# Kernel optimization log

Hardware: AMD Instinct MI355X
Metric: run time of the kernel (lower is better)

The kernel has to match this reference:

```python
import jax, jax.numpy as jnp
import numpy as np

NEG = -1e4      # BigBird additive mask value
LN_EPS = 1e-12  # BERT-style LayerNorm eps


def _bigbird_forward(xs_pad, mask, Wq, bq, Wk, bk, Wv, bv, Wo, bo, gamma, beta, rand_idx):
    b, n, hsz = xs_pad.shape
    H = rand_idx.shape[0]
    nb = rand_idx.shape[1] + 2          # one rand row per non-edge query block
    BS = n // nb                        # block size
    d = hsz // H
    r = rand_idx.shape[2]
    scale = 1.0 / np.sqrt(d).astype(np.float32)

    mf = mask.reshape(b, n).astype(xs_pad.dtype)   # (b,n) 1=token, 0=pad
    mb = mf.reshape(b, nb, BS)                     # blocked mask

    def proj(W, bias):
        return (xs_pad @ W + bias).reshape(b, n, H, d).transpose(0, 2, 1, 3)

    q = proj(Wq, bq) * scale            # (b,H,n,d)
    k = proj(Wk, bk)
    v = proj(Wv, bv)
    qb = q.reshape(b, H, nb, BS, d)
    kb = k.reshape(b, H, nb, BS, d)
    vb = v.reshape(b, H, nb, BS, d)

    # ---- global rows: first / last query block attend to all keys ----
    def full_row(qi):                   # qi: (b,H,BS,d)
        s = jnp.einsum('bhqd,bhkd->bhqk', qi, k) + (1.0 - mf)[:, None, None, :] * NEG
        return jnp.einsum('bhqk,bhkd->bhqd', jax.nn.softmax(s, axis=-1), v)

    ctx_first = full_row(qb[:, :, 0])
    ctx_last = full_row(qb[:, :, nb - 1])

    # ---- random key/value blocks: per-head, per-query-block gather ----
    hidx = jnp.arange(H)[:, None, None]
    rand_k = kb[:, hidx, rand_idx].reshape(b, H, nb - 2, r * BS, d)
    rand_v = vb[:, hidx, rand_idx].reshape(b, H, nb - 2, r * BS, d)
    rand_m = mb[:, rand_idx].reshape(b, H, nb - 2, r * BS)

    def sparse_row(qi, kc, vc, mc):     # kc:(b,H,K,d), mc:(b,H,K)
        s = jnp.einsum('bhqd,bhkd->bhqk', qi, kc) + (1.0 - mc)[:, :, None, :] * NEG
        return jnp.einsum('bhqk,bhkd->bhqd', jax.nn.softmax(s, axis=-1), vc)

    def gather_blocks(ids, ridx):
        kc = jnp.concatenate([kb[:, :, j] for j in ids] + [rand_k[:, :, ridx]], axis=2)
        vc = jnp.concatenate([vb[:, :, j] for j in ids] + [rand_v[:, :, ridx]], axis=2)
        mc = jnp.concatenate([jnp.broadcast_to(mb[:, None, j], (b, H, BS)) for j in ids]
                             + [rand_m[:, :, ridx]], axis=2)
        return kc, vc, mc

    # second / penultimate query blocks: window + globals + rand
    ctx_second = sparse_row(qb[:, :, 1], *gather_blocks([0, 1, 2, nb - 1], 0))
    ctx_penult = sparse_row(qb[:, :, nb - 2], *gather_blocks([nb - 3, nb - 2, nb - 1, 0], nb - 3))

    # ---- middle rows i in [2, nb-3]: 3-block sliding window + first/last global + r random ----
    nmid = nb - 4
    mid = jnp.arange(2, nb - 2)
    win = mid[:, None] + jnp.arange(-1, 2)[None, :]        # (nmid,3)
    k_win = kb[:, :, win].reshape(b, H, nmid, 3 * BS, d)
    v_win = vb[:, :, win].reshape(b, H, nmid, 3 * BS, d)
    m_win = jnp.broadcast_to(mb[:, win].reshape(b, 1, nmid, 3 * BS), (b, H, nmid, 3 * BS))

    def rep_glob(t):                     # (b,H,BS,...) -> (b,H,nmid,BS,...)
        return jnp.broadcast_to(t[:, :, None], (b, H, nmid) + t.shape[2:])

    k_mid = jnp.concatenate([k_win, rep_glob(kb[:, :, 0]), rep_glob(kb[:, :, nb - 1]),
                             rand_k[:, :, 1:nb - 3]], axis=3)
    v_mid = jnp.concatenate([v_win, rep_glob(vb[:, :, 0]), rep_glob(vb[:, :, nb - 1]),
                             rand_v[:, :, 1:nb - 3]], axis=3)
    m_first = jnp.broadcast_to(mb[:, None, None, 0], (b, H, nmid, BS))
    m_last = jnp.broadcast_to(mb[:, None, None, nb - 1], (b, H, nmid, BS))
    m_mid = jnp.concatenate([m_win, m_first, m_last, rand_m[:, :, 1:nb - 3]], axis=3)

    s_mid = jnp.einsum('bhmqd,bhmkd->bhmqk', qb[:, :, 2:nb - 2], k_mid) \
            + (1.0 - m_mid)[:, :, :, None, :] * NEG
    ctx_mid = jnp.einsum('bhmqk,bhmkd->bhmqd', jax.nn.softmax(s_mid, axis=-1), v_mid)

    ctx = jnp.concatenate([ctx_first[:, :, None], ctx_second[:, :, None], ctx_mid,
                           ctx_penult[:, :, None], ctx_last[:, :, None]], axis=2)
    ctx = ctx.reshape(b, H, n, d).transpose(0, 2, 1, 3).reshape(b, n, hsz)
    ctx = ctx * mf[:, :, None]           # from_mask on output rows

    # BigBirdSelfOutput: dense + residual + LayerNorm (dropout=0 / eval)
    y = ctx @ Wo + bo + xs_pad
    mu = y.mean(-1, keepdims=True)
    var = ((y - mu) ** 2).mean(-1, keepdims=True)
    return (y - mu) * jax.lax.rsqrt(var + LN_EPS) * gamma + beta


def setup_inputs() -> dict:
    key = jax.random.key(0)
    ks = jax.random.split(key, 6)
    B, N, HSZ, H, BS, R = 4, 4096, 1024, 16, 64, 3
    NB = N // BS
    init = lambda k, shp: jax.random.normal(k, shp, dtype=jnp.float32) * 0.02
    return {
        'xs_pad': jax.random.normal(ks[0], (B, N, HSZ), dtype=jnp.float32),
        'mask': jnp.ones((B, 1, N), dtype=jnp.int32),
        'Wq': init(ks[1], (HSZ, HSZ)), 'bq': jnp.zeros((HSZ,), jnp.float32),
        'Wk': init(ks[2], (HSZ, HSZ)), 'bk': jnp.zeros((HSZ,), jnp.float32),
        'Wv': init(ks[3], (HSZ, HSZ)), 'bv': jnp.zeros((HSZ,), jnp.float32),
        'Wo': init(ks[4], (HSZ, HSZ)), 'bo': jnp.zeros((HSZ,), jnp.float32),
        'gamma': jnp.ones((HSZ,), jnp.float32), 'beta': jnp.zeros((HSZ,), jnp.float32),
        'rand_idx': jax.random.randint(ks[5], (H, NB - 2, R), 1, NB - 1).astype(jnp.int32),
    }


def reference(xs_pad, mask, Wq, bq, Wk, bk, Wv, bv, Wo, bo, gamma, beta, rand_idx):
    return _bigbird_forward(xs_pad, mask, Wq, bq, Wk, bk, Wv, bv, Wo, bo, gamma, beta, rand_idx)
```

## Files before the change

kernel.cpp:

```cpp
#include <hip/hip_runtime.h>
#include <hip/hip_bf16.h>

#define B_   4
#define N_   4096
#define HSZ  1024
#define H_   16
#define D_   64
#define NB_  64
#define R_   3
#define M_   (B_*N_)
#define NEGV (-1e4f)
#define LOG2E 1.4426950408889634f

typedef float f32x4 __attribute__((ext_vector_type(4)));
typedef short s16x8 __attribute__((ext_vector_type(8)));
typedef __bf16 b16x8 __attribute__((ext_vector_type(8)));

__device__ __forceinline__ f32x4 mfma16(s16x8 a, s16x8 b, f32x4 c) {
  return __builtin_amdgcn_mfma_f32_16x16x32_bf16(
      __builtin_bit_cast(b16x8, a), __builtin_bit_cast(b16x8, b), c, 0, 0, 0);
}

__device__ __forceinline__ short f2b(float x) {
  __hip_bfloat16 h = __float2bfloat16(x);
  return (short)__builtin_bit_cast(unsigned short, h);
}

__device__ __forceinline__ unsigned pack2(float a, float b) {
  return (unsigned)(unsigned short)f2b(a) |
         ((unsigned)(unsigned short)f2b(b) << 16);
}

__device__ __forceinline__ void gl_lds16(const short* g, short* l) {
  __builtin_amdgcn_global_load_lds(
      (const __attribute__((address_space(1))) unsigned int*)g,
      (__attribute__((address_space(3))) unsigned int*)l, 16, 0, 0);
}

__global__ __launch_bounds__(256) void k_prep(const float* __restrict__ in,
                                              short* __restrict__ out,
                                              const float* __restrict__ Wq,
                                              const float* __restrict__ Wk,
                                              const float* __restrict__ Wv,
                                              const float* __restrict__ Wo,
                                              short* __restrict__ wt) {
  const int tid = threadIdx.x;
  if (blockIdx.x < 8192) {
    size_t i = ((size_t)blockIdx.x * 256 + tid) * 8;
    float4 a = *(const float4*)&in[i];
    float4 b = *(const float4*)&in[i + 4];
    s16x8 o;
    o[0] = f2b(a.x); o[1] = f2b(a.y); o[2] = f2b(a.z); o[3] = f2b(a.w);
    o[4] = f2b(b.x); o[5] = f2b(b.y); o[6] = f2b(b.z); o[7] = f2b(b.w);
    *(s16x8*)&out[i] = o;
    return;
  }
  const int bid = blockIdx.x - 8192;
  const int z = bid >> 8;
  const int rest = bid & 255;
  const int tk = (rest >> 4) * 64, tn = (rest & 15) * 64;
  const float* src = (z == 0) ? Wq : (z == 1) ? Wk : (z == 2) ? Wv : Wo;
  short* dst = wt + (size_t)z * HSZ * HSZ;
  __shared__ __align__(16) float t[64][68];
#pragma unroll
  for (int r = 0; r < 4; ++r) {
    int c = tid + r * 256;
    int row = c >> 4, seg = c & 15;
    *(float4*)&t[row][seg * 4] =
        *(const float4*)&src[(size_t)(tk + row) * HSZ + tn + seg * 4];
  }
  __syncthreads();
#pragma unroll
  for (int r = 0; r < 2; ++r) {
    int c = tid + r * 256;
    int row = c >> 3, seg = c & 7;
    s16x8 o;
#pragma unroll
    for (int u = 0; u < 8; ++u) o[u] = f2b(t[seg * 8 + u][row]);
    *(s16x8*)&dst[(size_t)(tn + row) * HSZ + tk + seg * 8] = o;
  }
}

template <bool SWAP>
__device__ __forceinline__ void gemm8_core(
    const short* __restrict__ A, const short* __restrict__ Bt, int tm, int tn,
    short (&a_lds)[2][256][64], short (&b_lds)[2][256][64],
    f32x4 (&acc)[8][4], int wave, int lane) {
  const int lq = lane & 15, g = lane >> 4;
  const int wm = wave >> 2, wn = wave & 3;
  const int sl8 = lane >> 3;
  const int sc = ((lane & 7) ^ sl8) * 8;

  auto ST_A = [&](int buf, int kt) {
#pragma unroll
    for (int h = 0; h < 2; ++h)
#pragma unroll
      for (int u = 0; u < 2; ++u) {
        const int rbase = h * 128 + wave * 8 + u * 64;
        gl_lds16(&A[(size_t)(tm + rbase + sl8) * HSZ + kt * 64 + sc],
                 &a_lds[buf][rbase][0]);
      }
  };
  auto ST_B = [&](int buf, int kt) {
#pragma unroll
    for (int h = 0; h < 2; ++h)
#pragma unroll
      for (int u = 0; u < 2; ++u) {
        const int rbase = h * 128 + wave * 8 + u * 64;
        gl_lds16(&Bt[(size_t)(tn + rbase + sl8) * HSZ + kt * 64 + sc],
                 &b_lds[buf][rbase][0]);
      }
  };

  s16x8 bf[4][2];
  auto LOADB = [&](int buf) {
#pragma unroll
    for (int j = 0; j < 4; ++j) {
      const int row = wn * 64 + j * 16 + lq;
#pragma unroll
      for (int kk = 0; kk < 2; ++kk)
        bf[j][kk] =
            *(const s16x8*)&b_lds[buf][row][((kk * 4 + g) ^ (lq & 7)) * 8];
    }
  };
  s16x8 afc[2][2], afn[2][2];
  auto LOADA = [&](int buf, int m0, s16x8 (&af)[2][2]) {
#pragma unroll
    for (int i = 0; i < 2; ++i) {
      const int row = wm * 128 + (m0 + i) * 16 + lq;
#pragma unroll
      for (int kk = 0; kk < 2; ++kk)
        af[i][kk] =
            *(const s16x8*)&a_lds[buf][row][((kk * 4 + g) ^ (lq & 7)) * 8];
    }
  };
  auto MF = [&](s16x8 (&af)[2][2], int m0) {
    __builtin_amdgcn_s_setprio(1);
#pragma unroll
    for (int i = 0; i < 2; ++i)
#pragma unroll
      for (int j = 0; j < 4; ++j)
#pragma unroll
        for (int kk = 0; kk < 2; ++kk)
          acc[m0 + i][j] = SWAP
                               ? mfma16(bf[j][kk], af[i][kk], acc[m0 + i][j])
                               : mfma16(af[i][kk], bf[j][kk], acc[m0 + i][j]);
    __builtin_amdgcn_s_setprio(0);
    __builtin_amdgcn_s_barrier();
  };

  ST_A(0, 0);
  ST_B(0, 0);
  ST_B(1, 1);

  for (int p = 0; p < 8; ++p) {
    const int t = 2 * p;
    ST_A(1, t + 1);
    asm volatile("s_waitcnt vmcnt(8)" ::: "memory");
    __builtin_amdgcn_s_barrier();
    LOADB(0);
    LOADA(0, 0, afc);
    LOADA(0, 2, afn);
    MF(afc, 0);
    if (t + 2 < 16) ST_B(0, t + 2);
    LOADA(0, 4, afc);
    MF(afn, 2);
    LOADA(0, 6, afn);
    MF(afc, 4);
    MF(afn, 6);
    if (t + 2 < 16) ST_A(0, t + 2);
    if (p < 7) {
      asm volatile("s_waitcnt vmcnt(8)" ::: "memory");
    } else {
      asm volatile("s_waitcnt vmcnt(0)" ::: "memory");
    }
    __builtin_amdgcn_s_barrier();
    LOADB(1);
    LOADA(1, 0, afc);
    LOADA(1, 2, afn);
    MF(afc, 0);
    if (t + 3 < 16) ST_B(1, t + 3);
    LOADA(1, 4, afc);
    MF(afn, 2);
    LOADA(1, 6, afn);
    MF(afc, 4);
    MF(afn, 6);
  }
}

__global__ __launch_bounds__(512) void k_qkv(
    const short* __restrict__ A, const short* __restrict__ WT,
    const float* __restrict__ bq, const float* __restrict__ bk,
    const float* __restrict__ bv, short* __restrict__ oq,
    short* __restrict__ ok, short* __restrict__ ovt) {
  const int orig = blockIdx.x;
  const int xcd = orig & 7, r = orig >> 3;
  const int combo = r >> 3, tml = r & 7;
  const int z = combo >> 2, tnl = combo & 3;
  const int tm = (xcd * 8 + tml) * 256, tn = tnl * 256;
  const short* Bt = WT + (size_t)z * HSZ * HSZ;

  __shared__ __align__(16) short a_lds[2][256][64];
  __shared__ __align__(16) short b_lds[2][256][64];

  const int tid = threadIdx.x, lane = tid & 63, wave = tid >> 6;
  const int lq = lane & 15, g = lane >> 4;
  const int wm = wave >> 2, wn = wave & 3;

  f32x4 acc[8][4] = {};

  if (z == 2) {
    gemm8_core<false>(A, Bt, tm, tn, a_lds, b_lds, acc, wave, lane);
#pragma unroll
    for (int j = 0; j < 4; ++j) {
      const int col = tn + wn * 64 + j * 16 + lq;
      const int hh = col >> 6, dd = col & 63;
      const float bi = bv[col];
#pragma unroll
      for (int i = 0; i < 8; ++i) {
        const int nrow = tm + wm * 128 + i * 16 + g * 4;
        const int bb = nrow >> 12, nn = nrow & (N_ - 1);
        uint2 w;
        w.x = pack2(acc[i][j][0] + bi, acc[i][j][1] + bi);
        w.y = pack2(acc[i][j][2] + bi, acc[i][j][3] + bi);
        *(uint2*)&ovt[(((size_t)bb * H_ + hh) * D_ + dd) * N_ + nn] = w;
      }
    }
  } else {
    gemm8_core<true>(A, Bt, tm, tn, a_lds, b_lds, acc, wave, lane);
    const float* bias = z ? bk : bq;
    short* outb = z ? ok : oq;
    const float alpha = z ? 1.0f : 0.125f * LOG2E;
#pragma unroll
    for (int i = 0; i < 8; ++i) {
      const int row = tm + wm * 128 + i * 16 + lq;
#pragma unroll
      for (int j = 0; j < 4; ++j) {
        const int colb = tn + wn * 64 + j * 16 + g * 4;
        const float4 bi = *(const float4*)&bias[colb];
        const int bb = row >> 12, nn = row & (N_ - 1);
        const int hh = colb >> 6, dd = colb & 63;
        uint2 w;
        w.x = pack2((acc[i][j][0] + bi.x) * alpha,
                    (acc[i][j][1] + bi.y) * alpha);
        w.y = pack2((acc[i][j][2] + bi.z) * alpha,
                    (acc[i][j][3] + bi.w) * alpha);
        *(uint2*)&outb[(((size_t)bb * H_ + hh) * N_ + nn) * D_ + dd] = w;
      }
    }
  }
}

__global__ __launch_bounds__(512) void k_out(
    const short* __restrict__ A, const short* __restrict__ WT,
    const float* __restrict__ bo, const float* __restrict__ xs,
    float* __restrict__ yout) {
  const short* Bt = WT + (size_t)3 * HSZ * HSZ;

  __shared__ __align__(16) short a_lds[2][256][64];
  __shared__ __align__(16) short b_lds[2][256][64];

  const int tid = threadIdx.x, lane = tid & 63, wave = tid >> 6;
  const int lq = lane & 15, g = lane >> 4;
  const int wm = wave >> 2, wn = wave & 3;
  const int orig = blockIdx.x;
  const int xcd = orig & 7, r = orig >> 3;
  const int tnl = r >> 3, tml = r & 7;
  const int tm = (xcd * 8 + tml) * 256, tn = tnl * 256;

  f32x4 acc[8][4] = {};
  gemm8_core<true>(A, Bt, tm, tn, a_lds, b_lds, acc, wave, lane);

#pragma unroll
  for (int i = 0; i < 8; ++i) {
    const int row = tm + wm * 128 + i * 16 + lq;
#pragma unroll
    for (int j = 0; j < 4; ++j) {
      const int colb = tn + wn * 64 + j * 16 + g * 4;
      const float4 bi = *(const float4*)&bo[colb];
      const size_t idx = (size_t)row * HSZ + colb;
      const float4 xv = *(const float4*)&xs[idx];
      float4 yv;
      yv.x = acc[i][j][0] + bi.x + xv.x;
      yv.y = acc[i][j][1] + bi.y + xv.y;
      yv.z = acc[i][j][2] + bi.z + xv.z;
      yv.w = acc[i][j][3] + bi.w + xv.w;
      *(float4*)&yout[idx] = yv;
    }
  }
}

__global__ __launch_bounds__(256) void k_attn(
    const short* __restrict__ Q, const short* __restrict__ K,
    const short* __restrict__ VT, const int* __restrict__ mask,
    const int* __restrict__ rnd, short* __restrict__ ctx,
    float* __restrict__ pO, float* __restrict__ pm, float* __restrict__ pl) {
  const int orig = blockIdx.x;
  const int swg = (orig & 7) * 624 + (orig >> 3);
  const int s = swg % 78;
  const int bh_i = swg / 78;
  const int h = bh_i & 15, b = bh_i >> 4;
  const int tid = threadIdx.x, lane = tid & 63, wave = tid >> 6;
  const int g = lane >> 4, lq = lane & 15;

  __shared__ __align__(16) short k_lds[2][64][64];
  __shared__ __align__(16) short vt_lds[2][64][64];
  __shared__ __align__(16) short p_lds[4][16][72];
  __shared__ __align__(16) float bias_s[8][64];
  __shared__ int list_s[8];
  __shared__ int Ls;

  const bool mid = (s < 62);
  const int qb = mid ? (s + 1) : (((s - 62) >> 3) ? (NB_ - 1) : 0);

  if (tid == 0) {
    int L;
    if (!mid) {
      int chunk = (s - 62) & 7;
#pragma unroll
      for (int i = 0; i < 8; ++i) list_s[i] = chunk * 8 + i;
      L = 8;
    } else {
      const int* rp = rnd + ((size_t)h * (NB_ - 2) + (qb - 1)) * R_;
      int n;
      if (qb == 1) {
        list_s[0] = 0; list_s[1] = 1; list_s[2] = 2; list_s[3] = NB_ - 1; n = 4;
      } else if (qb == NB_ - 2) {
        list_s[0] = NB_ - 3; list_s[1] = NB_ - 2; list_s[2] = NB_ - 1;
        list_s[3] = 0; n = 4;
      } else {
        list_s[0] = qb - 1; list_s[1] = qb; list_s[2] = qb + 1;
        list_s[3] = 0; list_s[4] = NB_ - 1; n = 5;
      }
      for (int j = 0; j < R_; ++j) list_s[n + j] = rp[j];
      L = n + R_;
      for (int i = L; i < 8; ++i) list_s[i] = 0;
    }
    Ls = L;
  }

  const size_t bh = (size_t)b * H_ + h;
  const size_t qrow = bh * N_ + (size_t)qb * 64 + wave * 16 + lq;
  s16x8 qf0 = *(const s16x8*)&Q[qrow * D_ + g * 8];
  s16x8 qf1 = *(const s16x8*)&Q[qrow * D_ + 32 + g * 8];

  __syncthreads();
  const int L = Ls;

  const int r0 = tid >> 3, sg = tid & 7;
  const int csl = (sg ^ (r0 & 7)) * 8;
  const int sw = (lq & 7);

  const short* Kb = K + bh * (size_t)N_ * D_;
  const short* Vb = VT + bh * (size_t)D_ * N_;
  const int* mb = mask + (size_t)b * N_;

  for (int t = tid; t < 512; t += 256) {
    const int i = t >> 6, kk2 = t & 63;
    bias_s[i][kk2] =
        (1.0f - (float)mb[list_s[i] * 64 + kk2]) * (NEGV * LOG2E);
  }

  s16x8 kr0, kr1, vr0, vr1;
  {
    const int kb = list_s[0];
    const short* kp = Kb + (size_t)kb * 64 * D_;
    const short* vp = Vb + (size_t)kb * 64;
    kr0 = *(const s16x8*)&kp[(size_t)r0 * D_ + sg * 8];
    kr1 = *(const s16x8*)&kp[(size_t)(r0 + 32) * D_ + sg * 8];
    vr0 = *(const s16x8*)&vp[(size_t)r0 * N_ + sg * 8];
    vr1 = *(const s16x8*)&vp[(size_t)(r0 + 32) * N_ + sg * 8];
  }

  s16x8 ones;
#pragma unroll
  for (int u = 0; u < 8; ++u) ones[u] = (short)0x3F80;

  f32x4 o[4] = {};
  f32x4 osum = {};
  float mshift = 0.0f;

  for (int it = 0; it < L; ++it) {
    const int buf = it & 1;
    *(s16x8*)&k_lds[buf][r0][csl] = kr0;
    *(s16x8*)&k_lds[buf][r0 + 32][csl] = kr1;
    *(s16x8*)&vt_lds[buf][r0][csl] = vr0;
    *(s16x8*)&vt_lds[buf][r0 + 32][csl] = vr1;
    if (it + 1 < L) {
      const int kb = list_s[it + 1];
      const short* kp = Kb + (size_t)kb * 64 * D_;
      const short* vp = Vb + (size_t)kb * 64;
      kr0 = *(const s16x8*)&kp[(size_t)r0 * D_ + sg * 8];
      kr1 = *(const s16x8*)&kp[(size_t)(r0 + 32) * D_ + sg * 8];
      vr0 = *(const s16x8*)&vp[(size_t)r0 * N_ + sg * 8];
      vr1 = *(const s16x8*)&vp[(size_t)(r0 + 32) * N_ + sg * 8];
    }
    __syncthreads();

    f32x4 st[4];
#pragma unroll
    for (int f = 0; f < 4; ++f) {
      f32x4 a0 = *(const f32x4*)&bias_s[it][f * 16 + g * 4];
      s16x8 af0 = *(const s16x8*)&k_lds[buf][f * 16 + lq][(g ^ sw) * 8];
      s16x8 af1 = *(const s16x8*)&k_lds[buf][f * 16 + lq][((4 + g) ^ sw) * 8];
      a0 = mfma16(af0, qf0, a0);
      a0 = mfma16(af1, qf1, a0);
      st[f] = a0;
    }

    if (mshift == 0.0f) {
#pragma unroll
      for (int f = 0; f < 4; ++f)
#pragma unroll
        for (int e = 0; e < 4; ++e) st[f][e] = exp2f(st[f][e]);
    } else {
#pragma unroll
      for (int f = 0; f < 4; ++f)
#pragma unroll
        for (int e = 0; e < 4; ++e) st[f][e] = exp2f(st[f][e] - mshift);
    }

#pragma unroll
    for (int f = 0; f < 4; ++f) {
      uint2 w = make_uint2(pack2(st[f][0], st[f][1]),
                           pack2(st[f][2], st[f][3]));
      *(uint2*)&p_lds[wave][lq][f * 16 + g * 4] = w;
    }

#pragma unroll
    for (int kk = 0; kk < 2; ++kk) {
      s16x8 pa = *(const s16x8*)&p_lds[wave][lq][kk * 32 + g * 8];
#pragma unroll
      for (int j = 0; j < 4; ++j) {
        s16x8 bv =
            *(const s16x8*)&vt_lds[buf][j * 16 + lq][((kk * 4 + g) ^ sw) * 8];
        o[j] = mfma16(pa, bv, o[j]);
      }
      osum = mfma16(pa, ones, osum);
    }

    float om = fmaxf(fmaxf(osum[0], osum[1]), fmaxf(osum[2], osum[3]));
    if (__any(om > 16777216.0f)) {
#pragma unroll
      for (int j = 0; j < 4; ++j) o[j] *= 5.9604645e-08f;
      osum *= 5.9604645e-08f;
      mshift += 24.0f;
    }
  }

  if (mid) {
    float rs[4];
#pragma unroll
    for (int e = 0; e < 4; ++e)
      rs[e] = (float)mb[qb * 64 + wave * 16 + g * 4 + e] /
              fmaxf(osum[e], 1e-30f);
    __syncthreads();
    short (*ost)[64] = k_lds[0];
#pragma unroll
    for (int j = 0; j < 4; ++j) {
      ost[wave * 16 + g * 4 + 0][j * 16 + lq] = f2b(o[j][0] * rs[0]);
      ost[wave * 16 + g * 4 + 1][j * 16 + lq] = f2b(o[j][1] * rs[1]);
      ost[wave * 16 + g * 4 + 2][j * 16 + lq] = f2b(o[j][2] * rs[2]);
      ost[wave * 16 + g * 4 + 3][j * 16 + lq] = f2b(o[j][3] * rs[3]);
    }
    __syncthreads();
#pragma unroll
    for (int pp = 0; pp < 2; ++pp) {
      int c = tid + pp * 256;
      int row = c >> 3, seg = c & 7;
      *(s16x8*)&ctx[((size_t)b * N_ + qb * 64 + row) * HSZ + h * D_ + seg * 8] =
          *(const s16x8*)&ost[row][seg * 8];
    }
  } else {
    const int e2 = s - 62;
    const int qsel = e2 >> 3, chunk = e2 & 7;
    const size_t eidx = (bh * 2 + qsel) * 8 + chunk;
    float* po = pO + eidx * 4096;
#pragma unroll
    for (int j = 0; j < 4; ++j)
#pragma unroll
      for (int e = 0; e < 4; ++e)
        po[(wave * 16 + g * 4 + e) * 64 + j * 16 + lq] = o[j][e];
    if (lq == 0) {
#pragma unroll
      for (int e = 0; e < 4; ++e) {
        pm[eidx * 64 + wave * 16 + g * 4 + e] = mshift;
        pl[eidx * 64 + wave * 16 + g * 4 + e] = osum[e];
      }
    }
  }
}

__global__ __launch_bounds__(256) void k_comb(
    const float* __restrict__ pO, const float* __restrict__ pm,
    const float* __restrict__ pl, const int* __restrict__ mask,
    short* __restrict__ ctx) {
  const int qsel = blockIdx.x, h = blockIdx.y, b = blockIdx.z;
  const int qb = qsel ? NB_ - 1 : 0;
  const int tid = threadIdx.x;
  const int q = tid >> 2, dq = tid & 3;
  const size_t base = (((size_t)b * H_ + h) * 2 + qsel) * 8;

  float mv[8];
  float M = -INFINITY;
#pragma unroll
  for (int i = 0; i < 8; ++i) {
    mv[i] = pm[(base + i) * 64 + q];
    M = fmaxf(M, mv[i]);
  }
  float Lsum = 0.0f;
#pragma unroll
  for (int i = 0; i < 8; ++i) {
    float w = exp2f(mv[i] - M);
    mv[i] = w;
    Lsum += pl[(base + i) * 64 + q] * w;
  }
  f32x4 acc[4] = {};
#pragma unroll
  for (int i = 0; i < 8; ++i) {
    const float* p = pO + (base + i) * 4096 + q * 64 + dq * 16;
    float w = mv[i];
#pragma unroll
    for (int u = 0; u < 4; ++u) {
      f32x4 v = *(const f32x4*)&p[u * 4];
      acc[u] += v * w;
    }
  }
  float sc = (float)mask[(size_t)b * N_ + qb * 64 + q] / fmaxf(Lsum, 1e-30f);
  s16x8 out0, out1;
#pragma unroll
  for (int u = 0; u < 8; ++u) {
    out0[u] = f2b(acc[u >> 2][u & 3] * sc);
    out1[u] = f2b(acc[2 + (u >> 2)][u & 3] * sc);
  }
  short* dst = &ctx[((size_t)b * N_ + qb * 64 + q) * HSZ + h * D_ + dq * 16];
  *(s16x8*)dst = out0;
  *(s16x8*)(dst + 8) = out1;
}

__global__ __launch_bounds__(256) void k_ln(float* __restrict__ y,
                                            const float* __restrict__ gamma,
                                            const float* __restrict__ beta) {
  const int row = blockIdx.x, tid = threadIdx.x, lane = tid & 63,
            wave = tid >> 6;
  __shared__ float s_sum[4], s_sq[4];
  float4 v = *(const float4*)&y[(size_t)row * HSZ + tid * 4];
  float s = v.x + v.y + v.z + v.w;
  float q = v.x * v.x + v.y * v.y + v.z * v.z + v.w * v.w;
#pragma unroll
  for (int m = 1; m <= 32; m <<= 1) {
    s += __shfl_xor(s, m);
    q += __shfl_xor(q, m);
  }
  if (lane == 0) { s_sum[wave] = s; s_sq[wave] = q; }
  __syncthreads();
  float S = s_sum[0] + s_sum[1] + s_sum[2] + s_sum[3];
  float Qs = s_sq[0] + s_sq[1] + s_sq[2] + s_sq[3];
  float mu = S * (1.0f / HSZ);
  float var = Qs * (1.0f / HSZ) - mu * mu;
  float r = rsqrtf(var + 1e-12f);
  float4 g = *(const float4*)&gamma[tid * 4];
  float4 be = *(const float4*)&beta[tid * 4];
  float4 outv;
  outv.x = (v.x - mu) * r * g.x + be.x;
  outv.y = (v.y - mu) * r * g.y + be.y;
  outv.z = (v.z - mu) * r * g.z + be.z;
  outv.w = (v.w - mu) * r * g.w + be.w;
  *(float4*)&y[(size_t)row * HSZ + tid * 4] = outv;
}

extern "C" void kernel_launch(void* const* d_in, const int* in_sizes, int n_in,
                              void* d_out, int out_size, void* d_ws,
                              size_t ws_size, hipStream_t stream) {
  const float* xs = (const float*)d_in[0];
  const int* mask = (const int*)d_in[1];
  const float* Wq = (const float*)d_in[2];
  const float* bq = (const float*)d_in[3];
  const float* Wk = (const float*)d_in[4];
  const float* bk = (const float*)d_in[5];
  const float* Wv = (const float*)d_in[6];
  const float* bv = (const float*)d_in[7];
  const float* Wo = (const float*)d_in[8];
  const float* bo = (const float*)d_in[9];
  const float* gamma = (const float*)d_in[10];
  const float* beta = (const float*)d_in[11];
  const int* rnd = (const int*)d_in[12];
  float* yout = (float*)d_out;

  char* ws = (char*)d_ws;
  const size_t SZ_XS = (size_t)M_ * HSZ * 2;
  const size_t SZ_WT = (size_t)4 * HSZ * HSZ * 2;
  short* xsb = (short*)ws;
  short* wt = (short*)(ws + SZ_XS);
  short* qbuf = (short*)(ws + SZ_XS + SZ_WT);
  short* kbuf = qbuf + (size_t)M_ * HSZ;
  short* vtb = kbuf + (size_t)M_ * HSZ;
  char* after = ws + SZ_XS + SZ_WT + 3 * SZ_XS;
  float* pO = (float*)(after + (1 << 20));
  float* pm = pO + (size_t)1024 * 4096;
  float* pl = pm + (size_t)1024 * 64;

  k_prep<<<9216, 256, 0, stream>>>(xs, xsb, Wq, Wk, Wv, Wo, wt);
  k_qkv<<<768, 512, 0, stream>>>(xsb, wt, bq, bk, bv, qbuf, kbuf, vtb);
  k_attn<<<4992, 256, 0, stream>>>(qbuf, kbuf, vtb, mask, rnd, xsb, pO, pm,
                                   pl);
  k_comb<<<dim3(2, H_, B_), 256, 0, stream>>>(pO, pm, pl, mask, xsb);
  k_out<<<256, 512, 0, stream>>>(xsb, wt, bo, xs, yout);
  k_ln<<<M_, 256, 0, stream>>>(yout, gamma, beta);
}
```

Before: 323.1 us.

## Stage sparse-attention K/V tiles with direct global-to-LDS async loads

Result: no change. 320.3 us (-0.9%).

```diff
diff --git a/kernel.cpp b/kernel.cpp
--- a/kernel.cpp
+++ b/kernel.cpp
@@ -347,9 +347,9 @@
   __syncthreads();
   const int L = Ls;
 
-  const int r0 = tid >> 3, sg = tid & 7;
-  const int csl = (sg ^ (r0 & 7)) * 8;
   const int sw = (lq & 7);
+  const int sl8 = lane >> 3;
+  const int scg = ((lane & 7) ^ sl8) * 8;
 
   const short* Kb = K + bh * (size_t)N_ * D_;
   const short* Vb = VT + bh * (size_t)D_ * N_;
@@ -360,17 +360,18 @@
     bias_s[i][kk2] =
         (1.0f - (float)mb[list_s[i] * 64 + kk2]) * (NEGV * LOG2E);
   }
-
-  s16x8 kr0, kr1, vr0, vr1;
-  {
-    const int kb = list_s[0];
+  asm volatile("s_waitcnt lgkmcnt(0)" ::: "memory");
+
+  auto STAGE = [&](int buf, int kb) {
     const short* kp = Kb + (size_t)kb * 64 * D_;
     const short* vp = Vb + (size_t)kb * 64;
-    kr0 = *(const s16x8*)&kp[(size_t)r0 * D_ + sg * 8];
-    kr1 = *(const s16x8*)&kp[(size_t)(r0 + 32) * D_ + sg * 8];
-    vr0 = *(const s16x8*)&vp[(size_t)r0 * N_ + sg * 8];
-    vr1 = *(const s16x8*)&vp[(size_t)(r0 + 32) * N_ + sg * 8];
-  }
+#pragma unroll
+    for (int u = 0; u < 2; ++u) {
+      const int rb = wave * 16 + u * 8;
+      gl_lds16(&kp[(size_t)(rb + sl8) * D_ + scg], &k_lds[buf][rb][0]);
+      gl_lds16(&vp[(size_t)(rb + sl8) * N_ + scg], &vt_lds[buf][rb][0]);
+    }
+  };
 
   s16x8 ones;
 #pragma unroll
@@ -380,22 +381,17 @@
   f32x4 osum = {};
   float mshift = 0.0f;
 
+  STAGE(0, list_s[0]);
+
   for (int it = 0; it < L; ++it) {
     const int buf = it & 1;
-    *(s16x8*)&k_lds[buf][r0][csl] = kr0;
-    *(s16x8*)&k_lds[buf][r0 + 32][csl] = kr1;
-    *(s16x8*)&vt_lds[buf][r0][csl] = vr0;
-    *(s16x8*)&vt_lds[buf][r0 + 32][csl] = vr1;
     if (it + 1 < L) {
-      const int kb = list_s[it + 1];
-      const short* kp = Kb + (size_t)kb * 64 * D_;
-      const short* vp = Vb + (size_t)kb * 64;
-      kr0 = *(const s16x8*)&kp[(size_t)r0 * D_ + sg * 8];
-      kr1 = *(const s16x8*)&kp[(size_t)(r0 + 32) * D_ + sg * 8];
-      vr0 = *(const s16x8*)&vp[(size_t)r0 * N_ + sg * 8];
-      vr1 = *(const s16x8*)&vp[(size_t)(r0 + 32) * N_ + sg * 8];
-    }
-    __syncthreads();
+      STAGE(buf ^ 1, list_s[it + 1]);
+      asm volatile("s_waitcnt vmcnt(4)" ::: "memory");
+    } else {
+      asm volatile("s_waitcnt vmcnt(0)" ::: "memory");
+    }
+    __builtin_amdgcn_s_barrier();
 
     f32x4 st[4];
 #pragma unroll
@@ -446,6 +442,7 @@
       osum *= 5.9604645e-08f;
       mshift += 24.0f;
     }
+    __builtin_amdgcn_s_barrier();
   }
 
   if (mid) {
```
